# Kernel optimization log

Measured on AMD Instinct MI355X. Metric: run time of the kernel, lower is better.

Reference implementation:

```python
import jax, jax.numpy as jnp
import numpy as np

N, E, C_IN, C_HID, C_OUT = 50000, 800000, 128, 64, 40


def _glorot(key, fan_in, fan_out):
    lim = np.sqrt(6.0 / (fan_in + fan_out)).astype(np.float32)
    return jax.random.uniform(key, (fan_in, fan_out), jnp.float32, -lim, lim)


def setup_inputs() -> dict:
    key = jax.random.key(0)
    kf, ks, ko, k1, k2 = jax.random.split(key, 5)
    features = jax.random.normal(kf, (N, C_IN), jnp.float32)
    src = jax.random.randint(ks, (E,), 0, N, jnp.int64 if jax.config.jax_enable_x64 else jnp.int32)
    # guarantee no self loops so add_remaining_self_loops == append full diagonal
    off = jax.random.randint(ko, (E,), 0, N - 1, src.dtype)
    dst = (src + 1 + off) % N
    return {
        "features": features,
        "src": src,
        "dst": dst,
        "W1": _glorot(k1, C_IN, C_HID),
        "b1": jnp.zeros((C_HID,), jnp.float32),
        "W2": _glorot(k2, C_HID, C_OUT),
        "b2": jnp.zeros((C_OUT,), jnp.float32),
    }


def reference(features, src, dst, W1, b1, W2, b2):
    n = features.shape[0]
    loop = jnp.arange(n, dtype=src.dtype)
    s = jnp.concatenate([src, loop])  # source nodes j (with self loops)
    d = jnp.concatenate([dst, loop])  # target nodes i
    ones = jnp.ones(s.shape[0], features.dtype)
    deg = jax.ops.segment_sum(ones, d, num_segments=n)  # in-degree incl. loop, >=1
    dinv = jax.lax.rsqrt(deg)
    norm = dinv[s] * dinv[d]  # D^{-1/2} A_hat D^{-1/2}, per edge

    def gcn_conv(x, W, b):
        h = x @ W  # [n, out]
        msgs = norm[:, None] * h[s]  # edge-wise gather + scale
        return jax.ops.segment_sum(msgs, d, num_segments=n) + b  # scatter-add

    x = jax.nn.relu(gcn_conv(features, W1, b1))
    # dropout: eval mode (training=False) -> identity
    x = gcn_conv(x, W2, b2)
    return jax.nn.log_softmax(x, axis=1)
```

## Files before the change

### kernel.cpp

```cpp
#include <hip/hip_runtime.h>
#include <math.h>

#define C_IN  128
#define C_HID 64
#define C_OUT 40
#define H1DW  32
#define H2DW  20

#define BKT_SH 7
#define BKT_N  (1 << BKT_SH)
#define CHUNK  1024
#define EPT    (CHUNK / 256)

__device__ __forceinline__ float bf2f(unsigned short u) {
    return __uint_as_float(((unsigned int)u) << 16);
}
__device__ __forceinline__ unsigned short f2bf(float f) {
    unsigned int x = __float_as_uint(f);
    return (unsigned short)((x + 0x7FFFu + ((x >> 16) & 1u)) >> 16);
}

__global__ void k_hist(const int* __restrict__ dst, int* __restrict__ hist2d, int e, int nbkt) {
    __shared__ int hist[512];
    for (int i = threadIdx.x; i < nbkt; i += 256) hist[i] = 0;
    __syncthreads();
    int base = blockIdx.x * CHUNK;
#pragma unroll
    for (int j = 0; j < EPT; ++j) {
        int i = base + j * 256 + threadIdx.x;
        if (i < e) atomicAdd(&hist[dst[i] >> BKT_SH], 1);
    }
    __syncthreads();
    int* row = hist2d + (size_t)blockIdx.x * nbkt;
    for (int i = threadIdx.x; i < nbkt; i += 256) row[i] = hist[i];
}

__global__ void k_bktscan(const int* __restrict__ hist2d, int* __restrict__ base2d,
                          int* __restrict__ tot, int nchunks, int nbkt) {
    __shared__ int wtot[4];
    const int b = blockIdx.x;
    const int t = threadIdx.x;
    const int lane = t & 63, wv = t >> 6;
    int carry = 0;
    for (int c0 = 0; c0 < nchunks; c0 += 256) {
        int c = c0 + t;
        int v = (c < nchunks) ? hist2d[(size_t)c * nbkt + b] : 0;
        int inc = v;
        for (int o = 1; o < 64; o <<= 1) { int u = __shfl_up(inc, o); if (lane >= o) inc += u; }
        if (lane == 63) wtot[wv] = inc;
        __syncthreads();
        int add = carry;
        for (int k = 0; k < wv; ++k) add += wtot[k];
        if (c < nchunks) base2d[(size_t)c * nbkt + b] = add + inc - v;
        carry += wtot[0] + wtot[1] + wtot[2] + wtot[3];
        __syncthreads();
    }
    if (t == 0) tot[b] = carry;
}

__global__ void k_scan_bkt(const int* __restrict__ tot, int* __restrict__ bstart, int nbkt, int e) {
    __shared__ int wtot[4];
    const int t = threadIdx.x;
    const int lane = t & 63, wv = t >> 6;
    int carry = 0;
    for (int b0 = 0; b0 < nbkt; b0 += 256) {
        int b = b0 + t;
        int v = (b < nbkt) ? tot[b] : 0;
        int inc = v;
        for (int o = 1; o < 64; o <<= 1) { int u = __shfl_up(inc, o); if (lane >= o) inc += u; }
        if (lane == 63) wtot[wv] = inc;
        __syncthreads();
        int add = carry;
        for (int k = 0; k < wv; ++k) add += wtot[k];
        if (b < nbkt) bstart[b] = add + inc - v;
        carry += wtot[0] + wtot[1] + wtot[2] + wtot[3];
        __syncthreads();
    }
    if (t == 0) bstart[nbkt] = e;
}

__global__ void k_binA(const int* __restrict__ src, const int* __restrict__ dst,
                       const int* __restrict__ bstart, const int* __restrict__ hist2d,
                       const int* __restrict__ base2d, unsigned int* __restrict__ bpack,
                       int e, int nbkt) {
    __shared__ int hist[512];
    __shared__ int excl[512];
    __shared__ int gbase[512];
    __shared__ int wtot[4];
    __shared__ unsigned int stage[CHUNK];
    const int t = threadIdx.x;
    const int base = blockIdx.x * CHUNK;
    const int lane = t & 63, wv = t >> 6;

    int carry = 0;
    for (int b0 = 0; b0 < nbkt; b0 += 256) {
        int b = b0 + t;
        int v = (b < nbkt) ? hist2d[(size_t)blockIdx.x * nbkt + b] : 0;
        int inc = v;
        for (int o = 1; o < 64; o <<= 1) { int u = __shfl_up(inc, o); if (lane >= o) inc += u; }
        if (lane == 63) wtot[wv] = inc;
        __syncthreads();
        int add = carry;
        for (int k = 0; k < wv; ++k) add += wtot[k];
        if (b < nbkt) {
            excl[b]  = add + inc - v;
            hist[b]  = 0;
            gbase[b] = bstart[b] + base2d[(size_t)blockIdx.x * nbkt + b];
        }
        carry += wtot[0] + wtot[1] + wtot[2] + wtot[3];
        __syncthreads();
    }

#pragma unroll
    for (int j = 0; j < EPT; ++j) {
        int i = base + j * 256 + t;
        if (i < e) {
            int d = dst[i];
            unsigned int pk = (unsigned int)src[i] | ((unsigned int)d << 16);
            int bk = d >> BKT_SH;
            int p  = excl[bk] + atomicAdd(&hist[bk], 1);
            stage[p] = pk;
        }
    }
    __syncthreads();

    int nchunk = min(CHUNK, e - base);
    for (int i = t; i < nchunk; i += 256) {
        unsigned int u = stage[i];
        int b = (int)(u >> 16) >> BKT_SH;
        bpack[gbase[b] + (i - excl[b])] = u;
    }
}

__global__ void k_binB(const int* __restrict__ bstart, const unsigned int* __restrict__ bpack,
                       int* __restrict__ row_start, float* __restrict__ dinv,
                       int* __restrict__ csr_src, int n, int e, int nbkt) {
    __shared__ int hist[BKT_N];
    __shared__ int excl[BKT_N];
    __shared__ int wtot[4];
    const int t = threadIdx.x;
    const int b = blockIdx.x;
    const int beg = bstart[b], end = bstart[b + 1];
    const int nodebase = b << BKT_SH;
    const int nloc = min(BKT_N, n - nodebase);

    for (int i = t; i < nloc; i += 256) hist[i] = 0;
    __syncthreads();
    for (int i = beg + t; i < end; i += 256)
        atomicAdd(&hist[(int)(bpack[i] >> 16) - nodebase], 1);
    __syncthreads();

    {
        int idx = t;
        int v = (idx < nloc) ? hist[idx] : 0;
        int inc = v; int lane = t & 63; int wv = t >> 6;
        for (int o = 1; o < 64; o <<= 1) { int u = __shfl_up(inc, o); if (lane >= o) inc += u; }
        if (lane == 63) wtot[wv] = inc;
        __syncthreads();
        int add = 0;
        for (int k = 0; k < wv; ++k) add += wtot[k];
        if (idx < nloc) excl[idx] = add + inc - v;
    }
    __syncthreads();

    for (int i = t; i < nloc; i += 256) {
        row_start[nodebase + i] = beg + excl[i];
        dinv[nodebase + i] = rsqrtf((float)hist[i] + 1.0f);
    }
    if (b == nbkt - 1 && t == 0) row_start[n] = e;
    __syncthreads();
    for (int i = t; i < nloc; i += 256) hist[i] = 0;
    __syncthreads();

    for (int i = beg + t; i < end; i += 256) {
        unsigned int u = bpack[i];
        int dl = (int)(u >> 16) - nodebase;
        int p = beg + excl[dl] + atomicAdd(&hist[dl], 1);
        csr_src[p] = (int)(u & 0xFFFFu);
    }
}

__global__ void k_gemm1(const float* __restrict__ X, const float* __restrict__ W1,
                        const float* __restrict__ dinv, unsigned short* __restrict__ h1b, int n) {
    __shared__ float xt[C_IN][64];
    __shared__ float wl[C_IN * C_HID];
    const int t = threadIdx.x;
    const int row0 = blockIdx.x * 64;

    for (int i = t; i < C_IN * C_HID; i += 256) wl[i] = W1[i];
    {
        int r = t >> 2, q = t & 3;
        int grow = row0 + r;
        for (int j = 0; j < 8; ++j) {
            int k = q * 32 + j * 4;
            float4 v = make_float4(0.f, 0.f, 0.f, 0.f);
            if (grow < n) v = *(const float4*)(X + (size_t)grow * C_IN + k);
            xt[k + 0][r] = v.x; xt[k + 1][r] = v.y; xt[k + 2][r] = v.z; xt[k + 3][r] = v.w;
        }
    }
    __syncthreads();

    const int rg = t >> 4, cg = t & 15;
    const int r0 = rg * 4, c0 = cg * 4;
    float acc[4][4] = {};
#pragma unroll 4
    for (int k = 0; k < C_IN; ++k) {
        float4 a = *(const float4*)&xt[k][r0];
        float4 b = *(const float4*)&wl[k * C_HID + c0];
        acc[0][0] = fmaf(a.x, b.x, acc[0][0]); acc[0][1] = fmaf(a.x, b.y, acc[0][1]);
        acc[0][2] = fmaf(a.x, b.z, acc[0][2]); acc[0][3] = fmaf(a.x, b.w, acc[0][3]);
        acc[1][0] = fmaf(a.y, b.x, acc[1][0]); acc[1][1] = fmaf(a.y, b.y, acc[1][1]);
        acc[1][2] = fmaf(a.y, b.z, acc[1][2]); acc[1][3] = fmaf(a.y, b.w, acc[1][3]);
        acc[2][0] = fmaf(a.z, b.x, acc[2][0]); acc[2][1] = fmaf(a.z, b.y, acc[2][1]);
        acc[2][2] = fmaf(a.z, b.z, acc[2][2]); acc[2][3] = fmaf(a.z, b.w, acc[2][3]);
        acc[3][0] = fmaf(a.w, b.x, acc[3][0]); acc[3][1] = fmaf(a.w, b.y, acc[3][1]);
        acc[3][2] = fmaf(a.w, b.z, acc[3][2]); acc[3][3] = fmaf(a.w, b.w, acc[3][3]);
    }
#pragma unroll
    for (int i = 0; i < 4; ++i) {
        int row = row0 + r0 + i;
        if (row < n) {
            float di = dinv[row];
            ushort4 o;
            o.x = f2bf(di * acc[i][0]); o.y = f2bf(di * acc[i][1]);
            o.z = f2bf(di * acc[i][2]); o.w = f2bf(di * acc[i][3]);
            *(ushort4*)(h1b + (size_t)row * C_HID + c0) = o;
        }
    }
}

__global__ void k_agg1g2(const int* __restrict__ row_start, const int* __restrict__ csr_src,
                         const unsigned short* __restrict__ h1b, const float* __restrict__ dinv,
                         const float* __restrict__ b1, const float* __restrict__ W2,
                         unsigned short* __restrict__ h2b, int n) {
    __shared__ float wl[C_HID * C_OUT];
    __shared__ float rowbuf[8][C_HID];
    const int t = threadIdx.x;
    for (int i = t; i < C_HID * C_OUT; i += 512) wl[i] = W2[i];
    __syncthreads();

    const int wid  = t >> 6;
    const int lane = t & 63;
    const int node = blockIdx.x * 8 + wid;
    if (node >= n) return;

    const int h  = lane >> 5;
    const int c2 = lane & 31;
    const unsigned int* h1d = (const unsigned int*)h1b;

    int beg = row_start[node], end = row_start[node + 1];
    float alo[4] = {0.f, 0.f, 0.f, 0.f}, ahi[4] = {0.f, 0.f, 0.f, 0.f};
    {
        unsigned int u = h1d[(size_t)node * H1DW + c2];
        if (h == 0) {
            alo[0] = __uint_as_float(u << 16);
            ahi[0] = __uint_as_float(u & 0xFFFF0000u);
        }
    }
    for (int j = beg; j < end; j += 64) {
        int sv = (j + lane < end) ? csr_src[j + lane] : 0;
        int m  = min(64, end - j);
        for (int k = 0; k < m; k += 8) {
#pragma unroll
            for (int i = 0; i < 4; ++i) {
                int idx = k + 2 * i + h;
                int s   = __shfl(sv, idx);
                float f = (idx < m) ? 1.f : 0.f;
                unsigned int u = h1d[(size_t)s * H1DW + c2];
                alo[i] = fmaf(f, __uint_as_float(u << 16), alo[i]);
                ahi[i] = fmaf(f, __uint_as_float(u & 0xFFFF0000u), ahi[i]);
            }
        }
    }
    float lo = (alo[0] + alo[1]) + (alo[2] + alo[3]);
    float hi = (ahi[0] + ahi[1]) + (ahi[2] + ahi[3]);
    lo += __shfl_xor(lo, 32);
    hi += __shfl_xor(hi, 32);

    float di = dinv[node];
    if (h == 0) {
        float2 bb = *(const float2*)(b1 + 2 * c2);
        float vlo = di * lo + bb.x;
        float vhi = di * hi + bb.y;
        rowbuf[wid][2 * c2]     = vlo > 0.f ? vlo : 0.f;
        rowbuf[wid][2 * c2 + 1] = vhi > 0.f ? vhi : 0.f;
    }
    if (lane < C_OUT) {
        float acc2 = 0.f;
#pragma unroll 8
        for (int k = 0; k < C_HID; ++k)
            acc2 = fmaf(rowbuf[wid][k], wl[k * C_OUT + lane], acc2);
        h2b[(size_t)node * C_OUT + lane] = f2bf(di * acc2);
    }
}

__global__ void k_agg2(const int* __restrict__ row_start, const int* __restrict__ csr_src,
                       const unsigned short* __restrict__ h2b, const float* __restrict__ dinv,
                       const float* __restrict__ b2, float* __restrict__ out, int n) {
    int node = (blockIdx.x * 256 + threadIdx.x) >> 6;
    int lane = threadIdx.x & 63;
    if (node >= n) return;
    const int h3 = lane / 20;
    const int c2 = lane - h3 * 20;
    const unsigned int* h2d = (const unsigned int*)h2b;

    int beg = row_start[node], end = row_start[node + 1];
    float alo[4] = {0.f, 0.f, 0.f, 0.f}, ahi[4] = {0.f, 0.f, 0.f, 0.f};
    if (h3 == 0) {
        unsigned int u = h2d[(size_t)node * H2DW + c2];
        alo[0] = __uint_as_float(u << 16);
        ahi[0] = __uint_as_float(u & 0xFFFF0000u);
    }
    for (int j = beg; j < end; j += 64) {
        int sv = (j + lane < end) ? csr_src[j + lane] : 0;
        int m = min(64, end - j);
        for (int k = 0; k < m; k += 12) {
#pragma unroll
            for (int i = 0; i < 4; ++i) {
                int idx = k + 3 * i + h3;
                int s = __shfl(sv, idx & 63);
                float f = (idx < m) ? 1.f : 0.f;
                unsigned int u = h2d[(size_t)s * H2DW + c2];
                alo[i] = fmaf(f, __uint_as_float(u << 16), alo[i]);
                ahi[i] = fmaf(f, __uint_as_float(u & 0xFFFF0000u), ahi[i]);
            }
        }
    }
    float lo = (alo[0] + alo[1]) + (alo[2] + alo[3]);
    float hi = (ahi[0] + ahi[1]) + (ahi[2] + ahi[3]);
    float lA = __shfl(lo, c2 + 20), lB = __shfl(lo, c2 + 40);
    float hA = __shfl(hi, c2 + 20), hB = __shfl(hi, c2 + 40);
    lo += lA + lB;
    hi += hA + hB;

    float di = dinv[node];
    float vlo = -INFINITY, vhi = -INFINITY, ex = 0.f;
    if (h3 == 0) {
        float2 bb = *(const float2*)(b2 + 2 * c2);
        vlo = di * lo + bb.x;
        vhi = di * hi + bb.y;
    }
    float mx = fmaxf(vlo, vhi);
    for (int off = 16; off; off >>= 1) mx = fmaxf(mx, __shfl_xor(mx, off));
    if (h3 == 0) ex = expf(vlo - mx) + expf(vhi - mx);
    float ss = ex;
    for (int off = 16; off; off >>= 1) ss += __shfl_xor(ss, off);
    float lse = mx + logf(ss);
    if (h3 == 0)
        *(float2*)(out + (size_t)node * C_OUT + 2 * c2) = make_float2(vlo - lse, vhi - lse);
}

extern "C" void kernel_launch(void* const* d_in, const int* in_sizes, int n_in,
                              void* d_out, int out_size, void* d_ws, size_t ws_size,
                              hipStream_t stream) {
    const float* X   = (const float*)d_in[0];
    const int*   src = (const int*)d_in[1];
    const int*   dst = (const int*)d_in[2];
    const float* W1  = (const float*)d_in[3];
    const float* b1  = (const float*)d_in[4];
    const float* W2  = (const float*)d_in[5];
    const float* b2  = (const float*)d_in[6];
    float* out = (float*)d_out;

    const int N = in_sizes[0] / C_IN;
    const int E = in_sizes[1];
    const int NBKT = (N + BKT_N - 1) >> BKT_SH;
    const int nchunks = (E + CHUNK - 1) / CHUNK;

    char* ws = (char*)d_ws;
    size_t off = 0;
    auto take = [&](size_t bytes) { char* p = ws + off; off = (off + bytes + 255) & ~(size_t)255; return p; };
    int*   hist2d    = (int*)  take((size_t)nchunks * NBKT * 4);
    int*   base2d    = (int*)  take((size_t)nchunks * NBKT * 4);
    int*   tot       = (int*)  take(512 * 4);
    int*   bstart    = (int*)  take(512 * 4);
    unsigned int* bpack = (unsigned int*)take((size_t)E * 4);
    int*   csr_src   = (int*)  take((size_t)E * 4);
    int*   row_start = (int*)  take((size_t)(N + 1) * 4);
    float* dinv      = (float*)take((size_t)N * 4);
    unsigned short* h1b = (unsigned short*)take((size_t)N * C_HID * 2);
    unsigned short* h2b = (unsigned short*)take((size_t)N * C_OUT * 2);

    k_hist    <<<nchunks, 256, 0, stream>>>(dst, hist2d, E, NBKT);
    k_bktscan <<<NBKT, 256, 0, stream>>>(hist2d, base2d, tot, nchunks, NBKT);
    k_scan_bkt<<<1, 256, 0, stream>>>(tot, bstart, NBKT, E);
    k_binA    <<<nchunks, 256, 0, stream>>>(src, dst, bstart, hist2d, base2d, bpack, E, NBKT);
    k_binB    <<<NBKT, 256, 0, stream>>>(bstart, bpack, row_start, dinv, csr_src, N, E, NBKT);

    k_gemm1   <<<(N + 63) / 64, 256, 0, stream>>>(X, W1, dinv, h1b, N);
    k_agg1g2  <<<(N + 7) / 8, 512, 0, stream>>>(row_start, csr_src, h1b, dinv, b1, W2, h2b, N);
    k_agg2    <<<((size_t)N * 64 + 255) / 256, 256, 0, stream>>>(row_start, csr_src, h2b, dinv, b2, out, N);
}
```

Measured before the change: 121.9 us.

## Split fused aggregation+GEMM2 into separate aggregation and register-tiled GEMM2 kernels

The fused layer-1 aggregation plus second matmul kernel is split in two. The aggregation kernel now writes relu'd bf16 activations and no longer loads W2 into 10KB of LDS per block, which should raise occupancy. A new GEMM2 kernel computes 96-row tiles with a 4x4 register tile instead of a per-lane serial dot product. The cost is an extra launch and an extra round trip of the N x 64 bf16 intermediate through global memory.

```diff
diff --git a/kernel.cpp b/kernel.cpp
--- a/kernel.cpp
+++ b/kernel.cpp
@@ -229,19 +229,13 @@
     }
 }
 
-__global__ void k_agg1g2(const int* __restrict__ row_start, const int* __restrict__ csr_src,
-                         const unsigned short* __restrict__ h1b, const float* __restrict__ dinv,
-                         const float* __restrict__ b1, const float* __restrict__ W2,
-                         unsigned short* __restrict__ h2b, int n) {
-    __shared__ float wl[C_HID * C_OUT];
-    __shared__ float rowbuf[8][C_HID];
-    const int t = threadIdx.x;
-    for (int i = t; i < C_HID * C_OUT; i += 512) wl[i] = W2[i];
-    __syncthreads();
-
+__global__ void k_agg1(const int* __restrict__ row_start, const int* __restrict__ csr_src,
+                       const unsigned short* __restrict__ h1b, const float* __restrict__ dinv,
+                       const float* __restrict__ b1, unsigned int* __restrict__ out1d, int n) {
+    const int t = threadIdx.x;
     const int wid  = t >> 6;
     const int lane = t & 63;
-    const int node = blockIdx.x * 8 + wid;
+    const int node = blockIdx.x * 4 + wid;
     if (node >= n) return;
 
     const int h  = lane >> 5;
@@ -277,20 +271,62 @@
     lo += __shfl_xor(lo, 32);
     hi += __shfl_xor(hi, 32);
 
-    float di = dinv[node];
     if (h == 0) {
+        float di = dinv[node];
         float2 bb = *(const float2*)(b1 + 2 * c2);
         float vlo = di * lo + bb.x;
         float vhi = di * hi + bb.y;
-        rowbuf[wid][2 * c2]     = vlo > 0.f ? vlo : 0.f;
-        rowbuf[wid][2 * c2 + 1] = vhi > 0.f ? vhi : 0.f;
-    }
-    if (lane < C_OUT) {
-        float acc2 = 0.f;
-#pragma unroll 8
-        for (int k = 0; k < C_HID; ++k)
-            acc2 = fmaf(rowbuf[wid][k], wl[k * C_OUT + lane], acc2);
-        h2b[(size_t)node * C_OUT + lane] = f2bf(di * acc2);
+        vlo = vlo > 0.f ? vlo : 0.f;
+        vhi = vhi > 0.f ? vhi : 0.f;
+        out1d[(size_t)node * H1DW + c2] =
+            (unsigned int)f2bf(vlo) | ((unsigned int)f2bf(vhi) << 16);
+    }
+}
+
+__global__ void k_gemm2(const unsigned int* __restrict__ out1d, const float* __restrict__ W2,
+                        const float* __restrict__ dinv, unsigned int* __restrict__ h2d, int n) {
+    __shared__ float xt[C_HID][96];
+    __shared__ float wl[C_HID * C_OUT];
+    const int t = threadIdx.x;
+    const int row0 = blockIdx.x * 96;
+
+    for (int i = t; i < C_HID * C_OUT; i += 256) wl[i] = W2[i];
+    for (int idx = t; idx < 96 * H1DW; idx += 256) {
+        int r = idx >> 5, d = idx & 31;
+        int grow = row0 + r;
+        unsigned int u = (grow < n) ? out1d[(size_t)grow * H1DW + d] : 0u;
+        xt[2 * d][r]     = __uint_as_float(u << 16);
+        xt[2 * d + 1][r] = __uint_as_float(u & 0xFFFF0000u);
+    }
+    __syncthreads();
+
+    if (t >= 240) return;
+    const int rg = t / 10, cg = t - rg * 10;
+    const int r0 = rg * 4, c0 = cg * 4;
+    float acc[4][4] = {};
+#pragma unroll 4
+    for (int k = 0; k < C_HID; ++k) {
+        float4 a = *(const float4*)&xt[k][r0];
+        float4 b = *(const float4*)&wl[k * C_OUT + c0];
+        acc[0][0] = fmaf(a.x, b.x, acc[0][0]); acc[0][1] = fmaf(a.x, b.y, acc[0][1]);
+        acc[0][2] = fmaf(a.x, b.z, acc[0][2]); acc[0][3] = fmaf(a.x, b.w, acc[0][3]);
+        acc[1][0] = fmaf(a.y, b.x, acc[1][0]); acc[1][1] = fmaf(a.y, b.y, acc[1][1]);
+        acc[1][2] = fmaf(a.y, b.z, acc[1][2]); acc[1][3] = fmaf(a.y, b.w, acc[1][3]);
+        acc[2][0] = fmaf(a.z, b.x, acc[2][0]); acc[2][1] = fmaf(a.z, b.y, acc[2][1]);
+        acc[2][2] = fmaf(a.z, b.z, acc[2][2]); acc[2][3] = fmaf(a.z, b.w, acc[2][3]);
+        acc[3][0] = fmaf(a.w, b.x, acc[3][0]); acc[3][1] = fmaf(a.w, b.y, acc[3][1]);
+        acc[3][2] = fmaf(a.w, b.z, acc[3][2]); acc[3][3] = fmaf(a.w, b.w, acc[3][3]);
+    }
+#pragma unroll
+    for (int i = 0; i < 4; ++i) {
+        int row = row0 + r0 + i;
+        if (row < n) {
+            float di = dinv[row];
+            unsigned int u0 = (unsigned int)f2bf(di * acc[i][0]) | ((unsigned int)f2bf(di * acc[i][1]) << 16);
+            unsigned int u1 = (unsigned int)f2bf(di * acc[i][2]) | ((unsigned int)f2bf(di * acc[i][3]) << 16);
+            h2d[(size_t)row * H2DW + (c0 >> 1)]     = u0;
+            h2d[(size_t)row * H2DW + (c0 >> 1) + 1] = u1;
+        }
     }
 }
 
@@ -378,8 +414,9 @@
     int*   csr_src   = (int*)  take((size_t)E * 4);
     int*   row_start = (int*)  take((size_t)(N + 1) * 4);
     float* dinv      = (float*)take((size_t)N * 4);
-    unsigned short* h1b = (unsigned short*)take((size_t)N * C_HID * 2);
-    unsigned short* h2b = (unsigned short*)take((size_t)N * C_OUT * 2);
+    unsigned short* h1b  = (unsigned short*)take((size_t)N * C_HID * 2);
+    unsigned int*   out1 = (unsigned int*)  take((size_t)N * H1DW * 4);
+    unsigned int*   h2d  = (unsigned int*)  take((size_t)N * H2DW * 4);
 
     k_hist    <<<nchunks, 256, 0, stream>>>(dst, hist2d, E, NBKT);
     k_bktscan <<<NBKT, 256, 0, stream>>>(hist2d, base2d, tot, nchunks, NBKT);
@@ -388,6 +425,8 @@
     k_binB    <<<NBKT, 256, 0, stream>>>(bstart, bpack, row_start, dinv, csr_src, N, E, NBKT);
 
     k_gemm1   <<<(N + 63) / 64, 256, 0, stream>>>(X, W1, dinv, h1b, N);
-    k_agg1g2  <<<(N + 7) / 8, 512, 0, stream>>>(row_start, csr_src, h1b, dinv, b1, W2, h2b, N);
-    k_agg2    <<<((size_t)N * 64 + 255) / 256, 256, 0, stream>>>(row_start, csr_src, h2b, dinv, b2, out, N);
-}
+    k_agg1    <<<(N + 3) / 4, 256, 0, stream>>>(row_start, csr_src, h1b, dinv, b1, out1, N);
+    k_gemm2   <<<(N + 95) / 96, 256, 0, stream>>>(out1, W2, dinv, h2d, N);
+    k_agg2    <<<((size_t)N * 64 + 255) / 256, 256, 0, stream>>>(row_start, csr_src,
+                                                                 (const unsigned short*)h2d, dinv, b2, out, N);
+}
```

New measurement: 123.9 us. About the same (+1.6%).

## Gather bf16 feature rows with 16-byte loads, padding h2 to 64 columns

Applied to the files above, without the earlier changes.

Both aggregation kernels now load neighbour rows as uint4 (8 bf16 per lane), so a wave processes 8 edges per step instead of 2–3. The cross-lane reduction becomes an xor-shuffle tree. The layer-2 hidden buffer is padded from 40 to 64 columns so rows align to 16 bytes, and the log-softmax is rewritten to use 5 lanes with 8 values each. This cuts per-edge load instructions and shuffles, at the cost of more bytes gathered per edge in layer 2 because of the padding.

```diff
diff --git a/kernel.cpp b/kernel.cpp
--- a/kernel.cpp
+++ b/kernel.cpp
@@ -4,17 +4,16 @@
 #define C_IN  128
 #define C_HID 64
 #define C_OUT 40
-#define H1DW  32
-#define H2DW  20
+#define H1Q   8
+#define H2Q   8
 
 #define BKT_SH 7
 #define BKT_N  (1 << BKT_SH)
 #define CHUNK  1024
 #define EPT    (CHUNK / 256)
 
-__device__ __forceinline__ float bf2f(unsigned short u) {
-    return __uint_as_float(((unsigned int)u) << 16);
-}
+__device__ __forceinline__ float bfLO(unsigned int u) { return __uint_as_float(u << 16); }
+__device__ __forceinline__ float bfHI(unsigned int u) { return __uint_as_float(u & 0xFFFF0000u); }
 __device__ __forceinline__ unsigned short f2bf(float f) {
     unsigned int x = __float_as_uint(f);
     return (unsigned short)((x + 0x7FFFu + ((x >> 16) & 1u)) >> 16);
@@ -230,7 +229,7 @@
 }
 
 __global__ void k_agg1g2(const int* __restrict__ row_start, const int* __restrict__ csr_src,
-                         const unsigned short* __restrict__ h1b, const float* __restrict__ dinv,
+                         const uint4* __restrict__ h1q, const float* __restrict__ dinv,
                          const float* __restrict__ b1, const float* __restrict__ W2,
                          unsigned short* __restrict__ h2b, int n) {
     __shared__ float wl[C_HID * C_OUT];
@@ -244,110 +243,135 @@
     const int node = blockIdx.x * 8 + wid;
     if (node >= n) return;
 
-    const int h  = lane >> 5;
-    const int c2 = lane & 31;
-    const unsigned int* h1d = (const unsigned int*)h1b;
+    const int h = lane >> 3;
+    const int q = lane & 7;
 
     int beg = row_start[node], end = row_start[node + 1];
     float alo[4] = {0.f, 0.f, 0.f, 0.f}, ahi[4] = {0.f, 0.f, 0.f, 0.f};
-    {
-        unsigned int u = h1d[(size_t)node * H1DW + c2];
-        if (h == 0) {
-            alo[0] = __uint_as_float(u << 16);
-            ahi[0] = __uint_as_float(u & 0xFFFF0000u);
-        }
+    if (h == 0) {
+        uint4 u = h1q[(size_t)node * H1Q + q];
+        alo[0] = bfLO(u.x); ahi[0] = bfHI(u.x);
+        alo[1] = bfLO(u.y); ahi[1] = bfHI(u.y);
+        alo[2] = bfLO(u.z); ahi[2] = bfHI(u.z);
+        alo[3] = bfLO(u.w); ahi[3] = bfHI(u.w);
     }
     for (int j = beg; j < end; j += 64) {
         int sv = (j + lane < end) ? csr_src[j + lane] : 0;
         int m  = min(64, end - j);
         for (int k = 0; k < m; k += 8) {
-#pragma unroll
-            for (int i = 0; i < 4; ++i) {
-                int idx = k + 2 * i + h;
-                int s   = __shfl(sv, idx);
-                float f = (idx < m) ? 1.f : 0.f;
-                unsigned int u = h1d[(size_t)s * H1DW + c2];
-                alo[i] = fmaf(f, __uint_as_float(u << 16), alo[i]);
-                ahi[i] = fmaf(f, __uint_as_float(u & 0xFFFF0000u), ahi[i]);
-            }
-        }
-    }
-    float lo = (alo[0] + alo[1]) + (alo[2] + alo[3]);
-    float hi = (ahi[0] + ahi[1]) + (ahi[2] + ahi[3]);
-    lo += __shfl_xor(lo, 32);
-    hi += __shfl_xor(hi, 32);
+            int   s = __shfl(sv, k + h);
+            float f = (k + h < m) ? 1.f : 0.f;
+            uint4 u = h1q[(size_t)s * H1Q + q];
+            alo[0] = fmaf(f, bfLO(u.x), alo[0]); ahi[0] = fmaf(f, bfHI(u.x), ahi[0]);
+            alo[1] = fmaf(f, bfLO(u.y), alo[1]); ahi[1] = fmaf(f, bfHI(u.y), ahi[1]);
+            alo[2] = fmaf(f, bfLO(u.z), alo[2]); ahi[2] = fmaf(f, bfHI(u.z), ahi[2]);
+            alo[3] = fmaf(f, bfLO(u.w), alo[3]); ahi[3] = fmaf(f, bfHI(u.w), ahi[3]);
+        }
+    }
+#pragma unroll
+    for (int off = 8; off <= 32; off <<= 1) {
+#pragma unroll
+        for (int i = 0; i < 4; ++i) {
+            alo[i] += __shfl_xor(alo[i], off);
+            ahi[i] += __shfl_xor(ahi[i], off);
+        }
+    }
 
     float di = dinv[node];
     if (h == 0) {
-        float2 bb = *(const float2*)(b1 + 2 * c2);
-        float vlo = di * lo + bb.x;
-        float vhi = di * hi + bb.y;
-        rowbuf[wid][2 * c2]     = vlo > 0.f ? vlo : 0.f;
-        rowbuf[wid][2 * c2 + 1] = vhi > 0.f ? vhi : 0.f;
+        float4 b0 = *(const float4*)(b1 + 8 * q);
+        float4 b4 = *(const float4*)(b1 + 8 * q + 4);
+        float v0 = fmaxf(fmaf(di, alo[0], b0.x), 0.f);
+        float v1 = fmaxf(fmaf(di, ahi[0], b0.y), 0.f);
+        float v2 = fmaxf(fmaf(di, alo[1], b0.z), 0.f);
+        float v3 = fmaxf(fmaf(di, ahi[1], b0.w), 0.f);
+        float v4 = fmaxf(fmaf(di, alo[2], b4.x), 0.f);
+        float v5 = fmaxf(fmaf(di, ahi[2], b4.y), 0.f);
+        float v6 = fmaxf(fmaf(di, alo[3], b4.z), 0.f);
+        float v7 = fmaxf(fmaf(di, ahi[3], b4.w), 0.f);
+        *(float4*)&rowbuf[wid][8 * q]     = make_float4(v0, v1, v2, v3);
+        *(float4*)&rowbuf[wid][8 * q + 4] = make_float4(v4, v5, v6, v7);
     }
     if (lane < C_OUT) {
         float acc2 = 0.f;
 #pragma unroll 8
         for (int k = 0; k < C_HID; ++k)
             acc2 = fmaf(rowbuf[wid][k], wl[k * C_OUT + lane], acc2);
-        h2b[(size_t)node * C_OUT + lane] = f2bf(di * acc2);
+        h2b[(size_t)node * 64 + lane] = f2bf(di * acc2);
+    } else {
+        h2b[(size_t)node * 64 + lane] = 0;
     }
 }
 
 __global__ void k_agg2(const int* __restrict__ row_start, const int* __restrict__ csr_src,
-                       const unsigned short* __restrict__ h2b, const float* __restrict__ dinv,
+                       const uint4* __restrict__ h2q, const float* __restrict__ dinv,
                        const float* __restrict__ b2, float* __restrict__ out, int n) {
     int node = (blockIdx.x * 256 + threadIdx.x) >> 6;
     int lane = threadIdx.x & 63;
     if (node >= n) return;
-    const int h3 = lane / 20;
-    const int c2 = lane - h3 * 20;
-    const unsigned int* h2d = (const unsigned int*)h2b;
+    const int h = lane >> 3;
+    const int q = lane & 7;
 
     int beg = row_start[node], end = row_start[node + 1];
     float alo[4] = {0.f, 0.f, 0.f, 0.f}, ahi[4] = {0.f, 0.f, 0.f, 0.f};
-    if (h3 == 0) {
-        unsigned int u = h2d[(size_t)node * H2DW + c2];
-        alo[0] = __uint_as_float(u << 16);
-        ahi[0] = __uint_as_float(u & 0xFFFF0000u);
+    if (h == 0) {
+        uint4 u = h2q[(size_t)node * H2Q + q];
+        alo[0] = bfLO(u.x); ahi[0] = bfHI(u.x);
+        alo[1] = bfLO(u.y); ahi[1] = bfHI(u.y);
+        alo[2] = bfLO(u.z); ahi[2] = bfHI(u.z);
+        alo[3] = bfLO(u.w); ahi[3] = bfHI(u.w);
     }
     for (int j = beg; j < end; j += 64) {
         int sv = (j + lane < end) ? csr_src[j + lane] : 0;
-        int m = min(64, end - j);
-        for (int k = 0; k < m; k += 12) {
-#pragma unroll
-            for (int i = 0; i < 4; ++i) {
-                int idx = k + 3 * i + h3;
-                int s = __shfl(sv, idx & 63);
-                float f = (idx < m) ? 1.f : 0.f;
-                unsigned int u = h2d[(size_t)s * H2DW + c2];
-                alo[i] = fmaf(f, __uint_as_float(u << 16), alo[i]);
-                ahi[i] = fmaf(f, __uint_as_float(u & 0xFFFF0000u), ahi[i]);
-            }
-        }
-    }
-    float lo = (alo[0] + alo[1]) + (alo[2] + alo[3]);
-    float hi = (ahi[0] + ahi[1]) + (ahi[2] + ahi[3]);
-    float lA = __shfl(lo, c2 + 20), lB = __shfl(lo, c2 + 40);
-    float hA = __shfl(hi, c2 + 20), hB = __shfl(hi, c2 + 40);
-    lo += lA + lB;
-    hi += hA + hB;
+        int m  = min(64, end - j);
+        for (int k = 0; k < m; k += 8) {
+            int   s = __shfl(sv, k + h);
+            float f = (k + h < m) ? 1.f : 0.f;
+            uint4 u = h2q[(size_t)s * H2Q + q];
+            alo[0] = fmaf(f, bfLO(u.x), alo[0]); ahi[0] = fmaf(f, bfHI(u.x), ahi[0]);
+            alo[1] = fmaf(f, bfLO(u.y), alo[1]); ahi[1] = fmaf(f, bfHI(u.y), ahi[1]);
+            alo[2] = fmaf(f, bfLO(u.z), alo[2]); ahi[2] = fmaf(f, bfHI(u.z), ahi[2]);
+            alo[3] = fmaf(f, bfLO(u.w), alo[3]); ahi[3] = fmaf(f, bfHI(u.w), ahi[3]);
+        }
+    }
+#pragma unroll
+    for (int off = 8; off <= 32; off <<= 1) {
+#pragma unroll
+        for (int i = 0; i < 4; ++i) {
+            alo[i] += __shfl_xor(alo[i], off);
+            ahi[i] += __shfl_xor(ahi[i], off);
+        }
+    }
 
     float di = dinv[node];
-    float vlo = -INFINITY, vhi = -INFINITY, ex = 0.f;
-    if (h3 == 0) {
-        float2 bb = *(const float2*)(b2 + 2 * c2);
-        vlo = di * lo + bb.x;
-        vhi = di * hi + bb.y;
-    }
-    float mx = fmaxf(vlo, vhi);
-    for (int off = 16; off; off >>= 1) mx = fmaxf(mx, __shfl_xor(mx, off));
-    if (h3 == 0) ex = expf(vlo - mx) + expf(vhi - mx);
-    float ss = ex;
-    for (int off = 16; off; off >>= 1) ss += __shfl_xor(ss, off);
-    float lse = mx + logf(ss);
-    if (h3 == 0)
-        *(float2*)(out + (size_t)node * C_OUT + 2 * c2) = make_float2(vlo - lse, vhi - lse);
+    float v0, v1, v2, v3, v4, v5, v6, v7;
+    float mloc = -INFINITY;
+    if (q < 5) {
+        float4 b0 = *(const float4*)(b2 + 8 * q);
+        float4 b4 = *(const float4*)(b2 + 8 * q + 4);
+        v0 = fmaf(di, alo[0], b0.x); v1 = fmaf(di, ahi[0], b0.y);
+        v2 = fmaf(di, alo[1], b0.z); v3 = fmaf(di, ahi[1], b0.w);
+        v4 = fmaf(di, alo[2], b4.x); v5 = fmaf(di, ahi[2], b4.y);
+        v6 = fmaf(di, alo[3], b4.z); v7 = fmaf(di, ahi[3], b4.w);
+        mloc = fmaxf(fmaxf(fmaxf(v0, v1), fmaxf(v2, v3)),
+                     fmaxf(fmaxf(v4, v5), fmaxf(v6, v7)));
+    }
+#pragma unroll
+    for (int off = 1; off <= 4; off <<= 1) mloc = fmaxf(mloc, __shfl_xor(mloc, off));
+    float es = 0.f;
+    if (q < 5) {
+        es = expf(v0 - mloc) + expf(v1 - mloc) + expf(v2 - mloc) + expf(v3 - mloc)
+           + expf(v4 - mloc) + expf(v5 - mloc) + expf(v6 - mloc) + expf(v7 - mloc);
+    }
+#pragma unroll
+    for (int off = 1; off <= 4; off <<= 1) es += __shfl_xor(es, off);
+    float lse = mloc + logf(es);
+    if (h == 0 && q < 5) {
+        *(float4*)(out + (size_t)node * C_OUT + 8 * q) =
+            make_float4(v0 - lse, v1 - lse, v2 - lse, v3 - lse);
+        *(float4*)(out + (size_t)node * C_OUT + 8 * q + 4) =
+            make_float4(v4 - lse, v5 - lse, v6 - lse, v7 - lse);
+    }
 }
 
 extern "C" void kernel_launch(void* const* d_in, const int* in_sizes, int n_in,
@@ -379,7 +403,7 @@
     int*   row_start = (int*)  take((size_t)(N + 1) * 4);
     float* dinv      = (float*)take((size_t)N * 4);
     unsigned short* h1b = (unsigned short*)take((size_t)N * C_HID * 2);
-    unsigned short* h2b = (unsigned short*)take((size_t)N * C_OUT * 2);
+    unsigned short* h2b = (unsigned short*)take((size_t)N * 64 * 2);
 
     k_hist    <<<nchunks, 256, 0, stream>>>(dst, hist2d, E, NBKT);
     k_bktscan <<<NBKT, 256, 0, stream>>>(hist2d, base2d, tot, nchunks, NBKT);
@@ -388,6 +412,8 @@
     k_binB    <<<NBKT, 256, 0, stream>>>(bstart, bpack, row_start, dinv, csr_src, N, E, NBKT);
 
     k_gemm1   <<<(N + 63) / 64, 256, 0, stream>>>(X, W1, dinv, h1b, N);
-    k_agg1g2  <<<(N + 7) / 8, 512, 0, stream>>>(row_start, csr_src, h1b, dinv, b1, W2, h2b, N);
-    k_agg2    <<<((size_t)N * 64 + 255) / 256, 256, 0, stream>>>(row_start, csr_src, h2b, dinv, b2, out, N);
-}
+    k_agg1g2  <<<(N + 7) / 8, 512, 0, stream>>>(row_start, csr_src, (const uint4*)h1b,
+                                                dinv, b1, W2, h2b, N);
+    k_agg2    <<<((size_t)N * 64 + 255) / 256, 256, 0, stream>>>(row_start, csr_src,
+                                                (const uint4*)h2b, dinv, b2, out, N);
+}
```

Result: slower. 133.4 us (+9.4%).

## Process multiple nodes per wavefront with prefetched CSR indices in aggregation kernels

Applied to the files above, without the earlier changes.

Both aggregation kernels now assign 8 consecutive nodes to each wavefront instead of one. Row offsets and dinv are loaded once per wave, and the neighbor index list for the next node is loaded ahead while the current node is processed. This amortizes per-node setup and the W2 shared-memory load in agg1g2 across more nodes, and hides csr_src load latency. The cost is 8x fewer waves, which lowers parallelism and latency hiding for the gathers, and more serial work per wave when degrees are uneven.

```diff
diff --git a/kernel.cpp b/kernel.cpp
--- a/kernel.cpp
+++ b/kernel.cpp
@@ -6,15 +6,15 @@
 #define C_OUT 40
 #define H1DW  32
 #define H2DW  20
+#define NPW   8
 
 #define BKT_SH 7
 #define BKT_N  (1 << BKT_SH)
 #define CHUNK  1024
 #define EPT    (CHUNK / 256)
 
-__device__ __forceinline__ float bf2f(unsigned short u) {
-    return __uint_as_float(((unsigned int)u) << 16);
-}
+__device__ __forceinline__ float bfLO(unsigned int u) { return __uint_as_float(u << 16); }
+__device__ __forceinline__ float bfHI(unsigned int u) { return __uint_as_float(u & 0xFFFF0000u); }
 __device__ __forceinline__ unsigned short f2bf(float f) {
     unsigned int x = __float_as_uint(f);
     return (unsigned short)((x + 0x7FFFu + ((x >> 16) & 1u)) >> 16);
@@ -241,113 +241,146 @@
 
     const int wid  = t >> 6;
     const int lane = t & 63;
-    const int node = blockIdx.x * 8 + wid;
-    if (node >= n) return;
+    const int node0 = (blockIdx.x * 8 + wid) * NPW;
+    if (node0 >= n) return;
 
     const int h  = lane >> 5;
     const int c2 = lane & 31;
     const unsigned int* h1d = (const unsigned int*)h1b;
 
-    int beg = row_start[node], end = row_start[node + 1];
-    float alo[4] = {0.f, 0.f, 0.f, 0.f}, ahi[4] = {0.f, 0.f, 0.f, 0.f};
-    {
-        unsigned int u = h1d[(size_t)node * H1DW + c2];
+    int rs = 0;
+    if (lane <= NPW) rs = row_start[min(node0 + lane, n)];
+    float dv = (lane < NPW) ? dinv[min(node0 + lane, n - 1)] : 0.f;
+
+    int b0 = __shfl(rs, 0), e0 = __shfl(rs, 1);
+    int sv_next = (b0 + lane < e0) ? csr_src[b0 + lane] : 0;
+
+    for (int i = 0; i < NPW; ++i) {
+        int node = node0 + i;
+        if (node >= n) break;
+        int beg = __shfl(rs, i), end = __shfl(rs, i + 1);
+        int sv = sv_next;
+        if (i + 1 < NPW) {
+            int b2 = __shfl(rs, i + 1), e2 = __shfl(rs, i + 2);
+            sv_next = (b2 + lane < e2) ? csr_src[b2 + lane] : 0;
+        }
+
+        float alo[4] = {0.f, 0.f, 0.f, 0.f}, ahi[4] = {0.f, 0.f, 0.f, 0.f};
+        {
+            unsigned int u = h1d[(size_t)node * H1DW + c2];
+            if (h == 0) { alo[0] = bfLO(u); ahi[0] = bfHI(u); }
+        }
+        for (int j = beg; j < end; j += 64) {
+            if (j > beg) sv = (j + lane < end) ? csr_src[j + lane] : 0;
+            int m = min(64, end - j);
+            for (int k = 0; k < m; k += 8) {
+#pragma unroll
+                for (int p = 0; p < 4; ++p) {
+                    int idx = k + 2 * p + h;
+                    int s   = __shfl(sv, idx);
+                    float f = (idx < m) ? 1.f : 0.f;
+                    unsigned int u = h1d[(size_t)s * H1DW + c2];
+                    alo[p] = fmaf(f, bfLO(u), alo[p]);
+                    ahi[p] = fmaf(f, bfHI(u), ahi[p]);
+                }
+            }
+        }
+        float lo = (alo[0] + alo[1]) + (alo[2] + alo[3]);
+        float hi = (ahi[0] + ahi[1]) + (ahi[2] + ahi[3]);
+        lo += __shfl_xor(lo, 32);
+        hi += __shfl_xor(hi, 32);
+
+        float di = __shfl(dv, i);
         if (h == 0) {
-            alo[0] = __uint_as_float(u << 16);
-            ahi[0] = __uint_as_float(u & 0xFFFF0000u);
-        }
-    }
-    for (int j = beg; j < end; j += 64) {
-        int sv = (j + lane < end) ? csr_src[j + lane] : 0;
-        int m  = min(64, end - j);
-        for (int k = 0; k < m; k += 8) {
-#pragma unroll
-            for (int i = 0; i < 4; ++i) {
-                int idx = k + 2 * i + h;
-                int s   = __shfl(sv, idx);
-                float f = (idx < m) ? 1.f : 0.f;
-                unsigned int u = h1d[(size_t)s * H1DW + c2];
-                alo[i] = fmaf(f, __uint_as_float(u << 16), alo[i]);
-                ahi[i] = fmaf(f, __uint_as_float(u & 0xFFFF0000u), ahi[i]);
-            }
-        }
-    }
-    float lo = (alo[0] + alo[1]) + (alo[2] + alo[3]);
-    float hi = (ahi[0] + ahi[1]) + (ahi[2] + ahi[3]);
-    lo += __shfl_xor(lo, 32);
-    hi += __shfl_xor(hi, 32);
-
-    float di = dinv[node];
-    if (h == 0) {
-        float2 bb = *(const float2*)(b1 + 2 * c2);
-        float vlo = di * lo + bb.x;
-        float vhi = di * hi + bb.y;
-        rowbuf[wid][2 * c2]     = vlo > 0.f ? vlo : 0.f;
-        rowbuf[wid][2 * c2 + 1] = vhi > 0.f ? vhi : 0.f;
-    }
-    if (lane < C_OUT) {
-        float acc2 = 0.f;
+            float2 bb = *(const float2*)(b1 + 2 * c2);
+            float vlo = fmaxf(fmaf(di, lo, bb.x), 0.f);
+            float vhi = fmaxf(fmaf(di, hi, bb.y), 0.f);
+            rowbuf[wid][2 * c2]     = vlo;
+            rowbuf[wid][2 * c2 + 1] = vhi;
+        }
+        if (lane < C_OUT) {
+            float acc2 = 0.f;
 #pragma unroll 8
-        for (int k = 0; k < C_HID; ++k)
-            acc2 = fmaf(rowbuf[wid][k], wl[k * C_OUT + lane], acc2);
-        h2b[(size_t)node * C_OUT + lane] = f2bf(di * acc2);
+            for (int k = 0; k < C_HID; ++k)
+                acc2 = fmaf(rowbuf[wid][k], wl[k * C_OUT + lane], acc2);
+            h2b[(size_t)node * C_OUT + lane] = f2bf(di * acc2);
+        }
     }
 }
 
 __global__ void k_agg2(const int* __restrict__ row_start, const int* __restrict__ csr_src,
                        const unsigned short* __restrict__ h2b, const float* __restrict__ dinv,
                        const float* __restrict__ b2, float* __restrict__ out, int n) {
-    int node = (blockIdx.x * 256 + threadIdx.x) >> 6;
-    int lane = threadIdx.x & 63;
-    if (node >= n) return;
+    const int t = threadIdx.x;
+    const int wid  = t >> 6;
+    const int lane = t & 63;
+    const int node0 = (blockIdx.x * 4 + wid) * NPW;
+    if (node0 >= n) return;
+
     const int h3 = lane / 20;
     const int c2 = lane - h3 * 20;
     const unsigned int* h2d = (const unsigned int*)h2b;
 
-    int beg = row_start[node], end = row_start[node + 1];
-    float alo[4] = {0.f, 0.f, 0.f, 0.f}, ahi[4] = {0.f, 0.f, 0.f, 0.f};
-    if (h3 == 0) {
-        unsigned int u = h2d[(size_t)node * H2DW + c2];
-        alo[0] = __uint_as_float(u << 16);
-        ahi[0] = __uint_as_float(u & 0xFFFF0000u);
-    }
-    for (int j = beg; j < end; j += 64) {
-        int sv = (j + lane < end) ? csr_src[j + lane] : 0;
-        int m = min(64, end - j);
-        for (int k = 0; k < m; k += 12) {
+    int rs = 0;
+    if (lane <= NPW) rs = row_start[min(node0 + lane, n)];
+    float dv = (lane < NPW) ? dinv[min(node0 + lane, n - 1)] : 0.f;
+
+    int b0 = __shfl(rs, 0), e0 = __shfl(rs, 1);
+    int sv_next = (b0 + lane < e0) ? csr_src[b0 + lane] : 0;
+
+    for (int i = 0; i < NPW; ++i) {
+        int node = node0 + i;
+        if (node >= n) break;
+        int beg = __shfl(rs, i), end = __shfl(rs, i + 1);
+        int sv = sv_next;
+        if (i + 1 < NPW) {
+            int bb2 = __shfl(rs, i + 1), ee2 = __shfl(rs, i + 2);
+            sv_next = (bb2 + lane < ee2) ? csr_src[bb2 + lane] : 0;
+        }
+
+        float alo[4] = {0.f, 0.f, 0.f, 0.f}, ahi[4] = {0.f, 0.f, 0.f, 0.f};
+        if (h3 == 0) {
+            unsigned int u = h2d[(size_t)node * H2DW + c2];
+            alo[0] = bfLO(u); ahi[0] = bfHI(u);
+        }
+        for (int j = beg; j < end; j += 64) {
+            if (j > beg) sv = (j + lane < end) ? csr_src[j + lane] : 0;
+            int m = min(64, end - j);
+            for (int k = 0; k < m; k += 12) {
 #pragma unroll
-            for (int i = 0; i < 4; ++i) {
-                int idx = k + 3 * i + h3;
-                int s = __shfl(sv, idx & 63);
-                float f = (idx < m) ? 1.f : 0.f;
-                unsigned int u = h2d[(size_t)s * H2DW + c2];
-                alo[i] = fmaf(f, __uint_as_float(u << 16), alo[i]);
-                ahi[i] = fmaf(f, __uint_as_float(u & 0xFFFF0000u), ahi[i]);
+                for (int p = 0; p < 4; ++p) {
+                    int idx = k + 3 * p + h3;
+                    int s = __shfl(sv, idx & 63);
+                    float f = (idx < m) ? 1.f : 0.f;
+                    unsigned int u = h2d[(size_t)s * H2DW + c2];
+                    alo[p] = fmaf(f, bfLO(u), alo[p]);
+                    ahi[p] = fmaf(f, bfHI(u), ahi[p]);
+                }
             }
         }
-    }
-    float lo = (alo[0] + alo[1]) + (alo[2] + alo[3]);
-    float hi = (ahi[0] + ahi[1]) + (ahi[2] + ahi[3]);
-    float lA = __shfl(lo, c2 + 20), lB = __shfl(lo, c2 + 40);
-    float hA = __shfl(hi, c2 + 20), hB = __shfl(hi, c2 + 40);
-    lo += lA + lB;
-    hi += hA + hB;
-
-    float di = dinv[node];
-    float vlo = -INFINITY, vhi = -INFINITY, ex = 0.f;
-    if (h3 == 0) {
-        float2 bb = *(const float2*)(b2 + 2 * c2);
-        vlo = di * lo + bb.x;
-        vhi = di * hi + bb.y;
-    }
-    float mx = fmaxf(vlo, vhi);
-    for (int off = 16; off; off >>= 1) mx = fmaxf(mx, __shfl_xor(mx, off));
-    if (h3 == 0) ex = expf(vlo - mx) + expf(vhi - mx);
-    float ss = ex;
-    for (int off = 16; off; off >>= 1) ss += __shfl_xor(ss, off);
-    float lse = mx + logf(ss);
-    if (h3 == 0)
-        *(float2*)(out + (size_t)node * C_OUT + 2 * c2) = make_float2(vlo - lse, vhi - lse);
+        float lo = (alo[0] + alo[1]) + (alo[2] + alo[3]);
+        float hi = (ahi[0] + ahi[1]) + (ahi[2] + ahi[3]);
+        float lA = __shfl(lo, c2 + 20), lB = __shfl(lo, c2 + 40);
+        float hA = __shfl(hi, c2 + 20), hB = __shfl(hi, c2 + 40);
+        lo += lA + lB;
+        hi += hA + hB;
+
+        float di = __shfl(dv, i);
+        float vlo = -INFINITY, vhi = -INFINITY, ex = 0.f;
+        if (h3 == 0) {
+            float2 bb = *(const float2*)(b2 + 2 * c2);
+            vlo = fmaf(di, lo, bb.x);
+            vhi = fmaf(di, hi, bb.y);
+        }
+        float mx = fmaxf(vlo, vhi);
+        for (int off = 16; off; off >>= 1) mx = fmaxf(mx, __shfl_xor(mx, off));
+        if (h3 == 0) ex = expf(vlo - mx) + expf(vhi - mx);
+        float ss = ex;
+        for (int off = 16; off; off >>= 1) ss += __shfl_xor(ss, off);
+        float lse = mx + logf(ss);
+        if (h3 == 0)
+            *(float2*)(out + (size_t)node * C_OUT + 2 * c2) = make_float2(vlo - lse, vhi - lse);
+    }
 }
 
 extern "C" void kernel_launch(void* const* d_in, const int* in_sizes, int n_in,
@@ -379,7 +412,7 @@
     int*   row_start = (int*)  take((size_t)(N + 1) * 4);
     float* dinv      = (float*)take((size_t)N * 4);
     unsigned short* h1b = (unsigned short*)take((size_t)N * C_HID * 2);
-    unsigned short* h2b = (unsigned short*)take((size_t)N * C_OUT * 2);
+    unsigned short* h2b = (unsigned short*)take((size_t)N * H2DW * 2 * 2);
 
     k_hist    <<<nchunks, 256, 0, stream>>>(dst, hist2d, E, NBKT);
     k_bktscan <<<NBKT, 256, 0, stream>>>(hist2d, base2d, tot, nchunks, NBKT);
@@ -388,6 +421,8 @@
     k_binB    <<<NBKT, 256, 0, stream>>>(bstart, bpack, row_start, dinv, csr_src, N, E, NBKT);
 
     k_gemm1   <<<(N + 63) / 64, 256, 0, stream>>>(X, W1, dinv, h1b, N);
-    k_agg1g2  <<<(N + 7) / 8, 512, 0, stream>>>(row_start, csr_src, h1b, dinv, b1, W2, h2b, N);
-    k_agg2    <<<((size_t)N * 64 + 255) / 256, 256, 0, stream>>>(row_start, csr_src, h2b, dinv, b2, out, N);
-}
+    k_agg1g2  <<<(N + 8 * NPW - 1) / (8 * NPW), 512, 0, stream>>>(row_start, csr_src, h1b,
+                                                                  dinv, b1, W2, h2b, N);
+    k_agg2    <<<(N + 4 * NPW - 1) / (4 * NPW), 256, 0, stream>>>(row_start, csr_src, h2b,
+                                                                  dinv, b2, out, N);
+}
```

Result: slower. 129.8 us (+6.5%).
